# Kernel tuning notes

Measured on AMD Instinct MI355X. Metric: run time of the kernel, lower is better.

## Reference

```python
import jax, jax.numpy as jnp
import numpy as np

H = 16  # num_heads; feature_dim = 1024, head dim d = 64

def _conv1(x, w, b):
    # kernel-size-1 Conv1d: pointwise channel mix on [B, F, N]
    return jnp.einsum('oi,bin->bon', w, x) + b[None, :, None]

def setup_inputs() -> dict:
    key = jax.random.key(0)
    ks = jax.random.split(key, 8)
    B, F, N = 2, 1024, 2048
    w = lambda k: jax.random.normal(k, (F, F), jnp.float32) * 0.02
    return {
        'query': jax.random.normal(ks[0], (B, F, N), jnp.float32),
        'key_':  jax.random.normal(ks[1], (B, F, N), jnp.float32),
        'value': jax.random.normal(ks[2], (B, F, N), jnp.float32),
        'wq': w(ks[3]), 'bq': jnp.zeros((F,), jnp.float32),
        'wk': w(ks[4]), 'bk': jnp.zeros((F,), jnp.float32),
        'wv': w(ks[5]), 'bv': jnp.zeros((F,), jnp.float32),
        'wm': w(ks[6]), 'bm': jnp.zeros((F,), jnp.float32),
    }

def reference(query, key_, value, wq, bq, wk, bk, wv, bv, wm, bm):
    B, F, N = query.shape
    d = F // H
    split = lambda x: x.reshape(B, d, H, N)  # matches torch .view(B, dim, heads, -1)
    q = split(_conv1(query, wq, bq))
    k = split(_conv1(key_, wk, bk))
    v = split(_conv1(value, wv, bv))
    scores = jnp.einsum('bdhn,bdhm->bhnm', q, k) / jnp.sqrt(jnp.float32(d))
    prob = jax.nn.softmax(scores, axis=-1)          # [B, H, N, M]
    x = jnp.einsum('bhnm,bdhm->bdhn', prob, v)      # [B, d, H, N]
    out = _conv1(x.reshape(B, F, N), wm, bm)        # merge
    return out, prob
```

## Files before the change

### kernel.cpp

```cpp
#include <hip/hip_runtime.h>
#include <cstdint>
#include <cstddef>

#define B_  2
#define F_  1024
#define N_  2048
#define H_  16
#define D_  64

typedef __attribute__((ext_vector_type(8))) __bf16 bf16x8;
typedef __attribute__((ext_vector_type(4))) float f32x4;

__device__ __forceinline__ unsigned short f2bf(float f) {
  union { float f; unsigned int u; } v; v.f = f;
  unsigned int r = v.u + 0x7FFFu + ((v.u >> 16) & 1u);
  return (unsigned short)(r >> 16);
}

__device__ __forceinline__ void gload16(const void* g, void* l) {
  __builtin_amdgcn_global_load_lds(
      (__attribute__((address_space(1))) void*)g,
      (__attribute__((address_space(3))) void*)l, 16, 0, 0);
}

__global__ __launch_bounds__(256) void k_transpose_cvt(
    const float* __restrict__ q, const float* __restrict__ k,
    const float* __restrict__ v, unsigned short* __restrict__ out)
{
  __shared__ float t[32][33];
  const int which = blockIdx.z >> 1;
  const int b = blockIdx.z & 1;
  const float* src = (which == 0) ? q : (which == 1) ? k : v;
  src += (size_t)b * (F_ * N_);
  unsigned short* dst = out + (size_t)which * ((size_t)B_ * N_ * F_) + (size_t)b * (N_ * F_);
  const int tid = threadIdx.x;
  const int r = tid >> 3, c4 = (tid & 7) << 2;
  float4 d = *(const float4*)(src + (size_t)(blockIdx.y * 32 + r) * N_ + blockIdx.x * 32 + c4);
  t[r][c4 + 0] = d.x; t[r][c4 + 1] = d.y; t[r][c4 + 2] = d.z; t[r][c4 + 3] = d.w;
  __syncthreads();
  unsigned long long pk =
      (unsigned long long)f2bf(t[c4 + 0][r]) |
      ((unsigned long long)f2bf(t[c4 + 1][r]) << 16) |
      ((unsigned long long)f2bf(t[c4 + 2][r]) << 32) |
      ((unsigned long long)f2bf(t[c4 + 3][r]) << 48);
  *(unsigned long long*)(dst + (size_t)(blockIdx.x * 32 + r) * F_ + blockIdx.y * 32 + c4) = pk;
}

__global__ __launch_bounds__(256) void k_cvt_weights(
    const float* __restrict__ wq, const float* __restrict__ wk,
    const float* __restrict__ wv, const float* __restrict__ wm,
    unsigned short* __restrict__ W2q, unsigned short* __restrict__ W2k,
    unsigned short* __restrict__ Wv2, unsigned short* __restrict__ Wm2)
{
  const int z = blockIdx.y;
  const int idx = (blockIdx.x * 256 + threadIdx.x) * 4;
  const int orow = idx >> 10;
  const int cb = idx & 1023;
  float a, b2, c, d2;
  unsigned short* dst;
  if (z <= 1) {
    const float* w = z ? wk : wq;
    const int o = ((orow & 63) << 4) | (orow >> 6);
    float4 d4 = *(const float4*)(w + (size_t)o * 1024 + cb);
    a = d4.x; b2 = d4.y; c = d4.z; d2 = d4.w;
    dst = z ? W2k : W2q;
  } else if (z == 2) {
    float4 d4 = *(const float4*)(wv + idx);
    a = d4.x; b2 = d4.y; c = d4.z; d2 = d4.w;
    dst = Wv2;
  } else {
    const float* wrow = wm + (size_t)orow * 1024;
    int f0 = cb;
    a  = wrow[((f0 & 63) << 4) | (f0 >> 6)]; f0++;
    b2 = wrow[((f0 & 63) << 4) | (f0 >> 6)]; f0++;
    c  = wrow[((f0 & 63) << 4) | (f0 >> 6)]; f0++;
    d2 = wrow[((f0 & 63) << 4) | (f0 >> 6)];
    dst = Wm2;
  }
  unsigned long long pk = (unsigned long long)f2bf(a) |
      ((unsigned long long)f2bf(b2) << 16) |
      ((unsigned long long)f2bf(c) << 32) |
      ((unsigned long long)f2bf(d2) << 48);
  *(unsigned long long*)(dst + idx) = pk;
}

__global__ __launch_bounds__(256) void k_gemm_bt(
    const unsigned short* __restrict__ A, const unsigned short* __restrict__ Bt,
    const float* __restrict__ bias, void* __restrict__ Cout,
    int mode, float scale)
{
  __shared__ __align__(16) char sA[16384];
  __shared__ __align__(16) char sB[16384];
  const int tid = threadIdx.x;
  const int l = tid & 63, w = tid >> 6;
  const int lr = l & 15, lg = l >> 4;
  const int bx = blockIdx.x, by = blockIdx.y, zb = blockIdx.z;
  const char* Ab = (const char*)A;
  const char* Bb = (const char*)Bt;
  if (mode == 0) Ab += (size_t)zb * ((size_t)N_ * F_ * 2);
  else           Bb += (size_t)zb * ((size_t)N_ * F_ * 2);
  const int wr = w >> 1, wc = w & 1;

  f32x4 acc[4][4];
  const f32x4 zero = {0.f, 0.f, 0.f, 0.f};
#pragma unroll
  for (int i = 0; i < 4; ++i)
#pragma unroll
    for (int j = 0; j < 4; ++j) acc[i][j] = zero;

  for (int kt = 0; kt < 16; ++kt) {
#pragma unroll
    for (int c = 0; c < 4; ++c) {
      const int D = c * 4096 + w * 1024 + l * 16;
      const int row = D >> 7, inner = D & 127;
      const int swz = inner ^ ((row & 7) << 4);
      gload16(Ab + ((size_t)(bx * 128 + row) * 1024 + kt * 64) * 2 + swz,
              sA + c * 4096 + w * 1024);
      gload16(Bb + ((size_t)(by * 128 + row) * 1024 + kt * 64) * 2 + swz,
              sB + c * 4096 + w * 1024);
    }
    __syncthreads();
#pragma unroll
    for (int kk = 0; kk < 2; ++kk) {
      bf16x8 af[4], bfv[4];
#pragma unroll
      for (int i = 0; i < 4; ++i) {
        const int row = wr * 64 + i * 16 + lr;
        af[i] = *(const bf16x8*)(sA + row * 128 + ((kk * 64 + lg * 16) ^ ((row & 7) << 4)));
      }
#pragma unroll
      for (int j = 0; j < 4; ++j) {
        const int row = wc * 64 + j * 16 + lr;
        bfv[j] = *(const bf16x8*)(sB + row * 128 + ((kk * 64 + lg * 16) ^ ((row & 7) << 4)));
      }
#pragma unroll
      for (int i = 0; i < 4; ++i)
#pragma unroll
        for (int j = 0; j < 4; ++j)
          acc[i][j] = __builtin_amdgcn_mfma_f32_16x16x32_bf16(af[i], bfv[j], acc[i][j], 0, 0, 0);
    }
    __syncthreads();
  }

#pragma unroll
  for (int i = 0; i < 4; ++i) {
#pragma unroll
    for (int j = 0; j < 4; ++j) {
      const int row0 = bx * 128 + wr * 64 + i * 16 + lg * 4;
      const int col = by * 128 + wc * 64 + j * 16 + lr;
#pragma unroll
      for (int r = 0; r < 4; ++r) {
        float v = acc[i][j][r];
        const int row = row0 + r;
        if (mode == 0) {
          v = (v + bias[((col & 63) << 4) | (col >> 6)]) * scale;
          ((unsigned short*)Cout)[(size_t)zb * 2097152 + (size_t)(col >> 6) * 131072 +
                                  (size_t)row * 64 + (col & 63)] = f2bf(v);
        } else if (mode == 1) {
          v += bias[row];
          ((unsigned short*)Cout)[(size_t)zb * 2097152 + (size_t)row * 2048 + col] = f2bf(v);
        } else {
          v += bias[row];
          ((float*)Cout)[(size_t)zb * 2097152 + (size_t)row * 2048 + col] = v;
        }
      }
    }
  }
}

__global__ __launch_bounds__(256) void k_attn(
    const unsigned short* __restrict__ Qt, const unsigned short* __restrict__ Kt,
    const unsigned short* __restrict__ Yv, float* __restrict__ prob,
    unsigned short* __restrict__ X2t)
{
  __shared__ __align__(16) char sK[16384];
  __shared__ __align__(16) char sV[16384];
  __shared__ __align__(16) char sP[16384];
  const int tid = threadIdx.x;
  const int l = tid & 63, w = tid >> 6;
  const int lr = l & 15, lg = l >> 4;
  const int qb = blockIdx.x, h = blockIdx.y, b = blockIdx.z;
  const int n0 = qb * 64 + w * 16;

  const char* Qh = (const char*)(Qt + (size_t)(b * 16 + h) * (2048 * 64));
  const char* Kh = (const char*)(Kt + (size_t)(b * 16 + h) * (2048 * 64));
  const char* Vh = (const char*)(Yv + (size_t)b * (1024 * 2048) + (size_t)h * 2048);
  float* probh = prob + (size_t)(b * 16 + h) * ((size_t)2048 * 2048);

  bf16x8 qf0 = *(const bf16x8*)(Qh + (size_t)(n0 + lr) * 128 + lg * 16);
  bf16x8 qf1 = *(const bf16x8*)(Qh + (size_t)(n0 + lr) * 128 + 64 + lg * 16);

  auto stage_k = [&](int mt) {
#pragma unroll
    for (int c = 0; c < 4; ++c) {
      const int D = c * 4096 + w * 1024 + l * 16;
      const int row = D >> 7, inner = D & 127;
      gload16(Kh + (size_t)(mt * 128 + row) * 128 + (inner ^ ((row & 7) << 4)),
              sK + c * 4096 + w * 1024);
    }
  };
  auto stage_v = [&](int mt) {
#pragma unroll
    for (int c = 0; c < 4; ++c) {
      const int D = c * 4096 + w * 1024 + l * 16;
      const int row = D >> 8, inner = D & 255;
      gload16(Vh + (size_t)row * 65536 + (size_t)mt * 256 + (inner ^ ((row & 15) << 4)),
              sV + c * 4096 + w * 1024);
    }
  };

  float mrun[4], lrun[4];
#pragma unroll
  for (int r = 0; r < 4; ++r) { mrun[r] = -1e30f; lrun[r] = 0.f; }

  for (int mt = 0; mt < 16; ++mt) {
    stage_k(mt);
    __syncthreads();
    f32x4 s[8];
    const f32x4 zero = {0.f, 0.f, 0.f, 0.f};
#pragma unroll
    for (int j = 0; j < 8; ++j) s[j] = zero;
#pragma unroll
    for (int kk = 0; kk < 2; ++kk) {
      bf16x8 qf = kk ? qf1 : qf0;
#pragma unroll
      for (int j = 0; j < 8; ++j) {
        const int row = j * 16 + lr;
        bf16x8 kf = *(const bf16x8*)(sK + row * 128 + ((kk * 64 + lg * 16) ^ ((row & 7) << 4)));
        s[j] = __builtin_amdgcn_mfma_f32_16x16x32_bf16(qf, kf, s[j], 0, 0, 0);
      }
    }
    __syncthreads();
#pragma unroll
    for (int r = 0; r < 4; ++r) {
      float m_ = s[0][r];
#pragma unroll
      for (int j = 1; j < 8; ++j) m_ = fmaxf(m_, s[j][r]);
#pragma unroll
      for (int d_ = 1; d_ < 16; d_ <<= 1) m_ = fmaxf(m_, __shfl_xor(m_, d_));
      const float mn = fmaxf(mrun[r], m_);
      float ps = 0.f;
#pragma unroll
      for (int j = 0; j < 8; ++j) ps += __expf(s[j][r] - mn);
#pragma unroll
      for (int d_ = 1; d_ < 16; d_ <<= 1) ps += __shfl_xor(ps, d_);
      lrun[r] = lrun[r] * __expf(mrun[r] - mn) + ps;
      mrun[r] = mn;
    }
  }

  float linv[4];
#pragma unroll
  for (int r = 0; r < 4; ++r) linv[r] = 1.f / lrun[r];

  f32x4 acc[4];
  {
    const f32x4 zero = {0.f, 0.f, 0.f, 0.f};
#pragma unroll
    for (int t = 0; t < 4; ++t) acc[t] = zero;
  }

  for (int mt = 0; mt < 16; ++mt) {
    stage_k(mt);
    stage_v(mt);
    __syncthreads();
    f32x4 s[8];
    const f32x4 zero = {0.f, 0.f, 0.f, 0.f};
#pragma unroll
    for (int j = 0; j < 8; ++j) s[j] = zero;
#pragma unroll
    for (int kk = 0; kk < 2; ++kk) {
      bf16x8 qf = kk ? qf1 : qf0;
#pragma unroll
      for (int j = 0; j < 8; ++j) {
        const int row = j * 16 + lr;
        bf16x8 kf = *(const bf16x8*)(sK + row * 128 + ((kk * 64 + lg * 16) ^ ((row & 7) << 4)));
        s[j] = __builtin_amdgcn_mfma_f32_16x16x32_bf16(qf, kf, s[j], 0, 0, 0);
      }
    }
#pragma unroll
    for (int j = 0; j < 8; ++j) {
#pragma unroll
      for (int r = 0; r < 4; ++r) {
        const float e = __expf(s[j][r] - mrun[r]) * linv[r];
        const int n_ = n0 + lg * 4 + r;
        probh[(size_t)n_ * 2048 + mt * 128 + j * 16 + lr] = e;
        const int nloc = w * 16 + lg * 4 + r;
        *(unsigned short*)(sP + nloc * 256 + (((j * 16 + lr) * 2) ^ ((nloc & 15) << 4))) = f2bf(e);
      }
    }
#pragma unroll
    for (int ks = 0; ks < 4; ++ks) {
      const int nr = w * 16 + lr;
      bf16x8 pa = *(const bf16x8*)(sP + nr * 256 + ((ks * 64 + lg * 16) ^ ((nr & 15) << 4)));
#pragma unroll
      for (int t = 0; t < 4; ++t) {
        const int vr = t * 16 + lr;
        bf16x8 vf = *(const bf16x8*)(sV + vr * 256 + ((ks * 64 + lg * 16) ^ ((vr & 15) << 4)));
        acc[t] = __builtin_amdgcn_mfma_f32_16x16x32_bf16(pa, vf, acc[t], 0, 0, 0);
      }
    }
    __syncthreads();
  }

#pragma unroll
  for (int t = 0; t < 4; ++t) {
#pragma unroll
    for (int r = 0; r < 4; ++r) {
      const int n_ = n0 + lg * 4 + r;
      X2t[((size_t)b * 2048 + n_) * 1024 + h * 64 + t * 16 + lr] = f2bf(acc[t][r]);
    }
  }
}

extern "C" void kernel_launch(void* const* d_in, const int* in_sizes, int n_in,
                              void* d_out, int out_size, void* d_ws, size_t ws_size,
                              hipStream_t stream)
{
  const float* query = (const float*)d_in[0];
  const float* key_  = (const float*)d_in[1];
  const float* value = (const float*)d_in[2];
  const float* wq = (const float*)d_in[3];
  const float* bq = (const float*)d_in[4];
  const float* wk = (const float*)d_in[5];
  const float* bk = (const float*)d_in[6];
  const float* wv = (const float*)d_in[7];
  const float* bv = (const float*)d_in[8];
  const float* wm = (const float*)d_in[9];
  const float* bm = (const float*)d_in[10];

  char* ws = (char*)d_ws;
  unsigned short* XT  = (unsigned short*)(ws);
  unsigned short* W2q = (unsigned short*)(ws + 25165824);
  unsigned short* W2k = (unsigned short*)(ws + 27262976);
  unsigned short* Wv2 = (unsigned short*)(ws + 29360128);
  unsigned short* Wm2 = (unsigned short*)(ws + 31457280);
  unsigned short* Qt  = (unsigned short*)(ws + 33554432);
  unsigned short* Kt  = (unsigned short*)(ws + 41943040);
  unsigned short* Yv  = (unsigned short*)(ws + 50331648);
  unsigned short* X2t = (unsigned short*)(ws + 58720256);

  unsigned short* XTq = XT;
  unsigned short* XTk = XT + 4194304;
  unsigned short* XTv = XT + 8388608;

  float* outp = (float*)d_out;
  float* prob = outp + 4194304;

  k_transpose_cvt<<<dim3(64, 32, 6), 256, 0, stream>>>(query, key_, value, XT);
  k_cvt_weights<<<dim3(1024, 4, 1), 256, 0, stream>>>(wq, wk, wv, wm, W2q, W2k, Wv2, Wm2);
  k_gemm_bt<<<dim3(16, 8, 2), 256, 0, stream>>>(XTq, W2q, bq, (void*)Qt, 0, 0.125f);
  k_gemm_bt<<<dim3(16, 8, 2), 256, 0, stream>>>(XTk, W2k, bk, (void*)Kt, 0, 1.0f);
  k_gemm_bt<<<dim3(8, 16, 2), 256, 0, stream>>>(Wv2, XTv, bv, (void*)Yv, 1, 1.0f);
  k_attn<<<dim3(32, 16, 2), 256, 0, stream>>>(Qt, Kt, Yv, prob, X2t);
  k_gemm_bt<<<dim3(8, 16, 2), 256, 0, stream>>>(Wm2, X2t, bm, (void*)outp, 2, 1.0f);
}
```

Baseline: 847.9 us.

## Double-buffer GEMM and attention K/V staging, shrink GEMM tiles, transpose score MFMA

```diff
diff --git a/kernel.cpp b/kernel.cpp
--- a/kernel.cpp
+++ b/kernel.cpp
@@ -6,10 +6,13 @@
 #define F_  1024
 #define N_  2048
 #define H_  16
-#define D_  64
 
 typedef __attribute__((ext_vector_type(8))) __bf16 bf16x8;
+typedef __attribute__((ext_vector_type(4))) __bf16 bf16x4;
 typedef __attribute__((ext_vector_type(4))) float f32x4;
+
+#define WAITV(n) asm volatile("s_waitcnt vmcnt(" n ")" ::: "memory")
+#define BAR() do { asm volatile("" ::: "memory"); __builtin_amdgcn_s_barrier(); asm volatile("" ::: "memory"); } while (0)
 
 __device__ __forceinline__ unsigned short f2bf(float f) {
   union { float f; unsigned int u; } v; v.f = f;
@@ -21,6 +24,10 @@
   __builtin_amdgcn_global_load_lds(
       (__attribute__((address_space(1))) void*)g,
       (__attribute__((address_space(3))) void*)l, 16, 0, 0);
+}
+
+__device__ __forceinline__ f32x4 vmax4(f32x4 x, f32x4 y) {
+  f32x4 r; r[0]=fmaxf(x[0],y[0]); r[1]=fmaxf(x[1],y[1]); r[2]=fmaxf(x[2],y[2]); r[3]=fmaxf(x[3],y[3]); return r;
 }
 
 __global__ __launch_bounds__(256) void k_transpose_cvt(
@@ -84,13 +91,13 @@
   *(unsigned long long*)(dst + idx) = pk;
 }
 
-__global__ __launch_bounds__(256) void k_gemm_bt(
+__global__ __launch_bounds__(256) void k_gemm64(
     const unsigned short* __restrict__ A, const unsigned short* __restrict__ Bt,
     const float* __restrict__ bias, void* __restrict__ Cout,
     int mode, float scale)
 {
-  __shared__ __align__(16) char sA[16384];
-  __shared__ __align__(16) char sB[16384];
+  __shared__ __align__(16) char sA[2][8192];
+  __shared__ __align__(16) char sB[2][8192];
   const int tid = threadIdx.x;
   const int l = tid & 63, w = tid >> 6;
   const int lr = l & 15, lg = l >> 4;
@@ -101,53 +108,61 @@
   else           Bb += (size_t)zb * ((size_t)N_ * F_ * 2);
   const int wr = w >> 1, wc = w & 1;
 
-  f32x4 acc[4][4];
+  f32x4 acc[2][2];
   const f32x4 zero = {0.f, 0.f, 0.f, 0.f};
 #pragma unroll
-  for (int i = 0; i < 4; ++i)
-#pragma unroll
-    for (int j = 0; j < 4; ++j) acc[i][j] = zero;
-
-  for (int kt = 0; kt < 16; ++kt) {
-#pragma unroll
-    for (int c = 0; c < 4; ++c) {
-      const int D = c * 4096 + w * 1024 + l * 16;
+  for (int i = 0; i < 2; ++i)
+#pragma unroll
+    for (int j = 0; j < 2; ++j) acc[i][j] = zero;
+
+  auto stage = [&](int kt, int bf) {
+#pragma unroll
+    for (int c = 0; c < 2; ++c) {
+      const int D = c * 4096 + tid * 16;
       const int row = D >> 7, inner = D & 127;
       const int swz = inner ^ ((row & 7) << 4);
-      gload16(Ab + ((size_t)(bx * 128 + row) * 1024 + kt * 64) * 2 + swz,
-              sA + c * 4096 + w * 1024);
-      gload16(Bb + ((size_t)(by * 128 + row) * 1024 + kt * 64) * 2 + swz,
-              sB + c * 4096 + w * 1024);
-    }
-    __syncthreads();
+      gload16(Ab + ((size_t)(bx * 64 + row) * 1024 + kt * 64) * 2 + swz,
+              &sA[bf][c * 4096 + w * 1024]);
+      gload16(Bb + ((size_t)(by * 64 + row) * 1024 + kt * 64) * 2 + swz,
+              &sB[bf][c * 4096 + w * 1024]);
+    }
+  };
+
+  stage(0, 0);
+  int buf = 0;
+  for (int kt = 0; kt < 16; ++kt) {
+    if (kt < 15) { stage(kt + 1, buf ^ 1); WAITV("4"); }
+    else         { WAITV("0"); }
+    BAR();
 #pragma unroll
     for (int kk = 0; kk < 2; ++kk) {
-      bf16x8 af[4], bfv[4];
-#pragma unroll
-      for (int i = 0; i < 4; ++i) {
-        const int row = wr * 64 + i * 16 + lr;
-        af[i] = *(const bf16x8*)(sA + row * 128 + ((kk * 64 + lg * 16) ^ ((row & 7) << 4)));
-      }
-#pragma unroll
-      for (int j = 0; j < 4; ++j) {
-        const int row = wc * 64 + j * 16 + lr;
-        bfv[j] = *(const bf16x8*)(sB + row * 128 + ((kk * 64 + lg * 16) ^ ((row & 7) << 4)));
-      }
-#pragma unroll
-      for (int i = 0; i < 4; ++i)
-#pragma unroll
-        for (int j = 0; j < 4; ++j)
+      bf16x8 af[2], bfv[2];
+#pragma unroll
+      for (int i = 0; i < 2; ++i) {
+        const int row = wr * 32 + i * 16 + lr;
+        af[i] = *(const bf16x8*)(&sA[buf][row * 128 + ((kk * 64 + lg * 16) ^ ((row & 7) << 4))]);
+      }
+#pragma unroll
+      for (int j = 0; j < 2; ++j) {
+        const int row = wc * 32 + j * 16 + lr;
+        bfv[j] = *(const bf16x8*)(&sB[buf][row * 128 + ((kk * 64 + lg * 16) ^ ((row & 7) << 4))]);
+      }
+#pragma unroll
+      for (int i = 0; i < 2; ++i)
+#pragma unroll
+        for (int j = 0; j < 2; ++j)
           acc[i][j] = __builtin_amdgcn_mfma_f32_16x16x32_bf16(af[i], bfv[j], acc[i][j], 0, 0, 0);
     }
-    __syncthreads();
-  }
-
-#pragma unroll
-  for (int i = 0; i < 4; ++i) {
-#pragma unroll
-    for (int j = 0; j < 4; ++j) {
-      const int row0 = bx * 128 + wr * 64 + i * 16 + lg * 4;
-      const int col = by * 128 + wc * 64 + j * 16 + lr;
+    BAR();
+    buf ^= 1;
+  }
+
+#pragma unroll
+  for (int i = 0; i < 2; ++i) {
+#pragma unroll
+    for (int j = 0; j < 2; ++j) {
+      const int row0 = bx * 64 + wr * 32 + i * 16 + lg * 4;
+      const int col = by * 64 + wc * 32 + j * 16 + lr;
 #pragma unroll
       for (int r = 0; r < 4; ++r) {
         float v = acc[i][j][r];
@@ -173,49 +188,50 @@
     const unsigned short* __restrict__ Yv, float* __restrict__ prob,
     unsigned short* __restrict__ X2t)
 {
-  __shared__ __align__(16) char sK[16384];
-  __shared__ __align__(16) char sV[16384];
+  __shared__ __align__(16) char sK[2][16384];
+  __shared__ __align__(16) char sV[2][16384];
   __shared__ __align__(16) char sP[16384];
   const int tid = threadIdx.x;
   const int l = tid & 63, w = tid >> 6;
   const int lr = l & 15, lg = l >> 4;
   const int qb = blockIdx.x, h = blockIdx.y, b = blockIdx.z;
-  const int n0 = qb * 64 + w * 16;
+  const int nl = qb * 64 + w * 16 + lr;
 
   const char* Qh = (const char*)(Qt + (size_t)(b * 16 + h) * (2048 * 64));
   const char* Kh = (const char*)(Kt + (size_t)(b * 16 + h) * (2048 * 64));
   const char* Vh = (const char*)(Yv + (size_t)b * (1024 * 2048) + (size_t)h * 2048);
-  float* probh = prob + (size_t)(b * 16 + h) * ((size_t)2048 * 2048);
-
-  bf16x8 qf0 = *(const bf16x8*)(Qh + (size_t)(n0 + lr) * 128 + lg * 16);
-  bf16x8 qf1 = *(const bf16x8*)(Qh + (size_t)(n0 + lr) * 128 + 64 + lg * 16);
-
-  auto stage_k = [&](int mt) {
+  float* probh = prob + (size_t)(b * 16 + h) * ((size_t)2048 * 2048) + (size_t)nl * 2048;
+
+  bf16x8 qf0 = *(const bf16x8*)(Qh + (size_t)nl * 128 + lg * 16);
+  bf16x8 qf1 = *(const bf16x8*)(Qh + (size_t)nl * 128 + 64 + lg * 16);
+
+  auto stage_k = [&](int mt, int bf) {
 #pragma unroll
     for (int c = 0; c < 4; ++c) {
       const int D = c * 4096 + w * 1024 + l * 16;
       const int row = D >> 7, inner = D & 127;
       gload16(Kh + (size_t)(mt * 128 + row) * 128 + (inner ^ ((row & 7) << 4)),
-              sK + c * 4096 + w * 1024);
+              &sK[bf][c * 4096 + w * 1024]);
     }
   };
-  auto stage_v = [&](int mt) {
+  auto stage_v = [&](int mt, int bf) {
 #pragma unroll
     for (int c = 0; c < 4; ++c) {
       const int D = c * 4096 + w * 1024 + l * 16;
       const int row = D >> 8, inner = D & 255;
       gload16(Vh + (size_t)row * 65536 + (size_t)mt * 256 + (inner ^ ((row & 15) << 4)),
-              sV + c * 4096 + w * 1024);
+              &sV[bf][c * 4096 + w * 1024]);
     }
   };
 
-  float mrun[4], lrun[4];
-#pragma unroll
-  for (int r = 0; r < 4; ++r) { mrun[r] = -1e30f; lrun[r] = 0.f; }
-
+  float mrun = -1e30f, lrun = 0.f;
+
+  stage_k(0, 0);
+  int buf = 0;
   for (int mt = 0; mt < 16; ++mt) {
-    stage_k(mt);
-    __syncthreads();
+    if (mt < 15) { stage_k(mt + 1, buf ^ 1); WAITV("4"); }
+    else         { WAITV("0"); }
+    BAR();
     f32x4 s[8];
     const f32x4 zero = {0.f, 0.f, 0.f, 0.f};
 #pragma unroll
@@ -226,32 +242,35 @@
 #pragma unroll
       for (int j = 0; j < 8; ++j) {
         const int row = j * 16 + lr;
-        bf16x8 kf = *(const bf16x8*)(sK + row * 128 + ((kk * 64 + lg * 16) ^ ((row & 7) << 4)));
-        s[j] = __builtin_amdgcn_mfma_f32_16x16x32_bf16(qf, kf, s[j], 0, 0, 0);
-      }
-    }
-    __syncthreads();
-#pragma unroll
-    for (int r = 0; r < 4; ++r) {
-      float m_ = s[0][r];
-#pragma unroll
-      for (int j = 1; j < 8; ++j) m_ = fmaxf(m_, s[j][r]);
-#pragma unroll
-      for (int d_ = 1; d_ < 16; d_ <<= 1) m_ = fmaxf(m_, __shfl_xor(m_, d_));
-      const float mn = fmaxf(mrun[r], m_);
-      float ps = 0.f;
-#pragma unroll
-      for (int j = 0; j < 8; ++j) ps += __expf(s[j][r] - mn);
-#pragma unroll
-      for (int d_ = 1; d_ < 16; d_ <<= 1) ps += __shfl_xor(ps, d_);
-      lrun[r] = lrun[r] * __expf(mrun[r] - mn) + ps;
-      mrun[r] = mn;
-    }
-  }
-
-  float linv[4];
-#pragma unroll
-  for (int r = 0; r < 4; ++r) linv[r] = 1.f / lrun[r];
+        bf16x8 kf = *(const bf16x8*)(&sK[buf][row * 128 + ((kk * 64 + lg * 16) ^ ((row & 7) << 4))]);
+        s[j] = __builtin_amdgcn_mfma_f32_16x16x32_bf16(kf, qf, s[j], 0, 0, 0);
+      }
+    }
+    BAR();
+    f32x4 a0 = vmax4(s[0], s[1]), a1 = vmax4(s[2], s[3]);
+    f32x4 a2 = vmax4(s[4], s[5]), a3 = vmax4(s[6], s[7]);
+    a0 = vmax4(a0, a1); a2 = vmax4(a2, a3); a0 = vmax4(a0, a2);
+    float mx = fmaxf(fmaxf(a0[0], a0[1]), fmaxf(a0[2], a0[3]));
+    mx = fmaxf(mx, __shfl_xor(mx, 16));
+    mx = fmaxf(mx, __shfl_xor(mx, 32));
+    const float mn = fmaxf(mrun, mx);
+    f32x4 ps4 = zero;
+#pragma unroll
+    for (int j = 0; j < 8; ++j) {
+      f32x4 e;
+#pragma unroll
+      for (int r = 0; r < 4; ++r) e[r] = __expf(s[j][r] - mn);
+      ps4 += e;
+    }
+    float ps = (ps4[0] + ps4[1]) + (ps4[2] + ps4[3]);
+    ps += __shfl_xor(ps, 16);
+    ps += __shfl_xor(ps, 32);
+    lrun = lrun * __expf(mrun - mn) + ps;
+    mrun = mn;
+    buf ^= 1;
+  }
+
+  const float linv = 1.f / lrun;
 
   f32x4 acc[4];
   {
@@ -260,10 +279,12 @@
     for (int t = 0; t < 4; ++t) acc[t] = zero;
   }
 
+  stage_k(0, 0); stage_v(0, 0);
+  buf = 0;
   for (int mt = 0; mt < 16; ++mt) {
-    stage_k(mt);
-    stage_v(mt);
-    __syncthreads();
+    if (mt < 15) { stage_k(mt + 1, buf ^ 1); stage_v(mt + 1, buf ^ 1); }
+    WAITV("8");
+    BAR();
     f32x4 s[8];
     const f32x4 zero = {0.f, 0.f, 0.f, 0.f};
 #pragma unroll
@@ -274,40 +295,42 @@
 #pragma unroll
       for (int j = 0; j < 8; ++j) {
         const int row = j * 16 + lr;
-        bf16x8 kf = *(const bf16x8*)(sK + row * 128 + ((kk * 64 + lg * 16) ^ ((row & 7) << 4)));
-        s[j] = __builtin_amdgcn_mfma_f32_16x16x32_bf16(qf, kf, s[j], 0, 0, 0);
+        bf16x8 kf = *(const bf16x8*)(&sK[buf][row * 128 + ((kk * 64 + lg * 16) ^ ((row & 7) << 4))]);
+        s[j] = __builtin_amdgcn_mfma_f32_16x16x32_bf16(kf, qf, s[j], 0, 0, 0);
       }
     }
 #pragma unroll
     for (int j = 0; j < 8; ++j) {
-#pragma unroll
-      for (int r = 0; r < 4; ++r) {
-        const float e = __expf(s[j][r] - mrun[r]) * linv[r];
-        const int n_ = n0 + lg * 4 + r;
-        probh[(size_t)n_ * 2048 + mt * 128 + j * 16 + lr] = e;
-        const int nloc = w * 16 + lg * 4 + r;
-        *(unsigned short*)(sP + nloc * 256 + (((j * 16 + lr) * 2) ^ ((nloc & 15) << 4))) = f2bf(e);
-      }
+      f32x4 e;
+#pragma unroll
+      for (int r = 0; r < 4; ++r) e[r] = __expf(s[j][r] - mrun) * linv;
+      float4 st; st.x = e[0]; st.y = e[1]; st.z = e[2]; st.w = e[3];
+      *(float4*)(probh + mt * 128 + j * 16 + lg * 4) = st;
+      bf16x4 pk;
+      pk[0] = (__bf16)e[0]; pk[1] = (__bf16)e[1]; pk[2] = (__bf16)e[2]; pk[3] = (__bf16)e[3];
+      const int gs = (j * 4 + lg) ^ ((lr & 7) << 1);
+      *(bf16x4*)(&sP[w * 4096 + lr * 256 + gs * 8]) = pk;
     }
 #pragma unroll
     for (int ks = 0; ks < 4; ++ks) {
-      const int nr = w * 16 + lr;
-      bf16x8 pa = *(const bf16x8*)(sP + nr * 256 + ((ks * 64 + lg * 16) ^ ((nr & 15) << 4)));
+      const int g0 = (ks * 8 + lg * 2) ^ ((lr & 7) << 1);
+      bf16x8 pa = *(const bf16x8*)(&sP[w * 4096 + lr * 256 + g0 * 8]);
 #pragma unroll
       for (int t = 0; t < 4; ++t) {
         const int vr = t * 16 + lr;
-        bf16x8 vf = *(const bf16x8*)(sV + vr * 256 + ((ks * 64 + lg * 16) ^ ((vr & 15) << 4)));
+        bf16x8 vf = *(const bf16x8*)(&sV[buf][vr * 256 + ((ks * 64 + lg * 16) ^ ((vr & 15) << 4))]);
         acc[t] = __builtin_amdgcn_mfma_f32_16x16x32_bf16(pa, vf, acc[t], 0, 0, 0);
       }
     }
-    __syncthreads();
+    BAR();
+    buf ^= 1;
   }
 
 #pragma unroll
   for (int t = 0; t < 4; ++t) {
 #pragma unroll
     for (int r = 0; r < 4; ++r) {
-      const int n_ = n0 + lg * 4 + r;
+      const int n_ = qb * 64 + w * 16 + lg * 4 + r;
       X2t[((size_t)b * 2048 + n_) * 1024 + h * 64 + t * 16 + lr] = f2bf(acc[t][r]);
     }
   }
@@ -349,9 +372,9 @@
 
   k_transpose_cvt<<<dim3(64, 32, 6), 256, 0, stream>>>(query, key_, value, XT);
   k_cvt_weights<<<dim3(1024, 4, 1), 256, 0, stream>>>(wq, wk, wv, wm, W2q, W2k, Wv2, Wm2);
-  k_gemm_bt<<<dim3(16, 8, 2), 256, 0, stream>>>(XTq, W2q, bq, (void*)Qt, 0, 0.125f);
-  k_gemm_bt<<<dim3(16, 8, 2), 256, 0, stream>>>(XTk, W2k, bk, (void*)Kt, 0, 1.0f);
-  k_gemm_bt<<<dim3(8, 16, 2), 256, 0, stream>>>(Wv2, XTv, bv, (void*)Yv, 1, 1.0f);
+  k_gemm64<<<dim3(32, 16, 2), 256, 0, stream>>>(XTq, W2q, bq, (void*)Qt, 0, 0.125f);
+  k_gemm64<<<dim3(32, 16, 2), 256, 0, stream>>>(XTk, W2k, bk, (void*)Kt, 0, 1.0f);
+  k_gemm64<<<dim3(16, 32, 2), 256, 0, stream>>>(Wv2, XTv, bv, (void*)Yv, 1, 1.0f);
   k_attn<<<dim3(32, 16, 2), 256, 0, stream>>>(Qt, Kt, Yv, prob, X2t);
-  k_gemm_bt<<<dim3(8, 16, 2), 256, 0, stream>>>(Wm2, X2t, bm, (void*)outp, 2, 1.0f);
-}
+  k_gemm64<<<dim3(16, 32, 2), 256, 0, stream>>>(Wm2, X2t, bm, (void*)outp, 2, 1.0f);
+}
```

New measurement: 789.2 us. -6.9%, faster.
